# Kernel optimization log

Hardware: AMD Instinct MI355X
Metric: run time of the kernel (lower is better)

Reference implementation:

```python
import jax, jax.numpy as jnp
import numpy as np

B, D_IN, H, DIM, K = 16384, 2000, 500, 64, 256
DELTA = -5.0


def _xavier(key, shape):
    fan_out, fan_in = shape
    lim = jnp.sqrt(6.0 / (fan_in + fan_out))
    return jax.random.uniform(key, shape, jnp.float32, -lim, lim)


def setup_inputs() -> dict:
    key = jax.random.key(0)
    ks = jax.random.split(key, 8)
    return {
        "epoch": 0,
        "pre_iter": 0,
        "x": jax.random.uniform(ks[0], (B, D_IN), jnp.float32),
        "mu": jax.random.normal(ks[1], (K, DIM), jnp.float32),
        "enc_w1": _xavier(ks[2], (H, D_IN)), "enc_b1": jnp.zeros((H,), jnp.float32),
        "enc_w2": _xavier(ks[3], (DIM, H)), "enc_b2": jnp.zeros((DIM,), jnp.float32),
        "fc0_w": _xavier(ks[4], (DIM, 2 * DIM)), "fc0_b": jnp.zeros((DIM,), jnp.float32),
        "dec_w1": _xavier(ks[5], (H, DIM)), "dec_b1": jnp.zeros((H,), jnp.float32),
        "dec_w2": _xavier(ks[6], (D_IN, H)), "dec_b2": jnp.zeros((D_IN,), jnp.float32),
    }


def reference(epoch, pre_iter, x, mu, enc_w1, enc_b1, enc_w2, enc_b2,
              fc0_w, fc0_b, dec_w1, dec_b1, dec_w2, dec_b2):
    # encoder (Dropout is identity in eval)
    h = jax.nn.relu(x @ enc_w1.T + enc_b1)            # [B, 500]
    z = h @ enc_w2.T + enc_b2                          # [B, dim]
    # Stein_IMG clustering step (mu is detached in the original)
    mu_d = jax.lax.stop_gradient(mu)
    diff = z[:, None, :] - mu_d[None, :, :]           # [B, K, dim]
    z_dist = jnp.mean(diff * diff, axis=2)            # [B, K]
    gamma = jax.nn.softmax(DELTA * z_dist, axis=1)    # [B, K]
    idx = jnp.argmax(gamma, axis=1)                   # [B]
    # one-hot scatter + matmul with mu == gather of nearest centroid
    quantized = mu_d[idx]                             # [B, dim]
    double_z = jnp.concatenate([z, quantized], axis=1)  # [B, 2*dim]
    recon_z = double_z @ fc0_w.T + fc0_b              # [B, dim]
    # decoder
    h2 = jax.nn.relu(recon_z @ dec_w1.T + dec_b1)     # [B, 500]
    recon_x = jax.nn.sigmoid(h2 @ dec_w2.T + dec_b2)  # [B, 2000]
    return (z, quantized, gamma, recon_x)
```

## Files before the change

kernel.cpp:

```cpp
#include <hip/hip_runtime.h>
#include <stdint.h>
#include <math.h>

#define NB   16384
#define DIN  2000
#define NH   500
#define ND   64
#define NKC  256

#define FLAG_CAP 4096
#define GAP_THR  0.002f

typedef __attribute__((ext_vector_type(4))) float  f32x4;
typedef __attribute__((ext_vector_type(4))) double f64x4;
typedef __attribute__((ext_vector_type(8))) short  s16x8;

__device__ __forceinline__ unsigned short f2bf_rne(float v) {
  unsigned int u = __float_as_uint(v);
  u += 0x7fffu + ((u >> 16) & 1u);
  return (unsigned short)(u >> 16);
}
__device__ __forceinline__ void split_rtz(float v, unsigned short &hi, unsigned short &lo) {
  unsigned int u = __float_as_uint(v);
  hi = (unsigned short)(u >> 16);
  float r = v - __uint_as_float(u & 0xffff0000u);
  lo = (unsigned short)(__float_as_uint(r) >> 16);
}

typedef const __attribute__((address_space(1))) void* gas_t;
typedef __attribute__((address_space(3))) void* las_t;
__device__ __forceinline__ void gl_lds16(const void* g, void* l) {
  __builtin_amdgcn_global_load_lds((gas_t)g, (las_t)l, 16, 0, 0);
}

__device__ __forceinline__ void split_pad_seg(const float* __restrict__ in,
                                              unsigned short* __restrict__ hi,
                                              unsigned short* __restrict__ lo,
                                              int R, int C, int Cp, int total,
                                              int bseg, int nblk) {
  int stride = nblk * 256;
  for (int idx = bseg * 256 + threadIdx.x; idx < total; idx += stride) {
    int r = idx / Cp, c = idx - r * Cp;
    float v = (r < R && c < C) ? in[(size_t)r * C + c] : 0.f;
    if (lo) {
      unsigned short h, l; split_rtz(v, h, l);
      hi[idx] = h; lo[idx] = l;
    } else {
      hi[idx] = f2bf_rne(v);
    }
  }
}

__global__ __launch_bounds__(256) void k_prep(const float* __restrict__ x,
                                              unsigned short* __restrict__ XHI,
                                              unsigned short* __restrict__ XLO,
                                              const float* __restrict__ w1,
                                              unsigned short* __restrict__ W1HI,
                                              unsigned short* __restrict__ W1LO,
                                              const float* __restrict__ w2,
                                              unsigned short* __restrict__ W2HI,
                                              unsigned short* __restrict__ W2LO,
                                              const float* __restrict__ dw1,
                                              unsigned short* __restrict__ DW1,
                                              const float* __restrict__ dw2,
                                              unsigned short* __restrict__ DW2,
                                              int* __restrict__ fcnt)
{
  const int b = blockIdx.x;
  if (b == 0 && threadIdx.x == 0) *fcnt = 0;
  if (b < 2048) {
    const int total = NB * 256;
    for (int idx = b * 256 + threadIdx.x; idx < total; idx += 2048 * 256) {
      int r = idx >> 8;
      int c8 = (idx & 255) << 3;
      s16x8 h8 = {0,0,0,0,0,0,0,0}, l8 = {0,0,0,0,0,0,0,0};
      if (c8 < DIN) {
        const float* src = x + (size_t)r * DIN + c8;
        f32x4 v0 = *(const f32x4*)src;
        f32x4 v1 = *(const f32x4*)(src + 4);
#pragma unroll
        for (int j = 0; j < 4; ++j) {
          unsigned short h, l;
          split_rtz(v0[j], h, l); h8[j] = (short)h; l8[j] = (short)l;
          split_rtz(v1[j], h, l); h8[4 + j] = (short)h; l8[4 + j] = (short)l;
        }
      }
      *(s16x8*)&XHI[(size_t)idx * 8] = h8;
      *(s16x8*)&XLO[(size_t)idx * 8] = l8;
    }
  } else if (b < 3072) {
    split_pad_seg(w1, W1HI, W1LO, 500, 2000, 2048, 512 * 2048, b - 2048, 1024);
  } else if (b < 3136) {
    split_pad_seg(w2, W2HI, W2LO, 64, 500, 512, 64 * 512, b - 3072, 64);
  } else if (b < 3200) {
    split_pad_seg(dw1, DW1, nullptr, 500, 64, 64, 512 * 64, b - 3136, 64);
  } else {
    split_pad_seg(dw2, DW2, nullptr, 2000, 500, 512, 2048 * 512, b - 3200, 896);
  }
}

template<int WR, int BN, int WC, bool SPLIT, int EPI>
__global__ __launch_bounds__(256) void k_gemm(
    const unsigned short* __restrict__ Ahi, const unsigned short* __restrict__ Alo,
    const unsigned short* __restrict__ Bhi, const unsigned short* __restrict__ Blo,
    const float* __restrict__ bias, int bias_n,
    void* __restrict__ out0, void* __restrict__ out1,
    int ldA, int K, int out_ld, int store_n)
{
  constexpr int BM = WR * 32, BK = 32;
  constexpr int ACH = BM * 4;
  constexpr int BCH = BN * 4;
  __shared__ unsigned short aHi[BM * BK];
  __shared__ unsigned short aLo[SPLIT ? BM * BK : 8];
  __shared__ unsigned short bHi[BN * BK];
  __shared__ unsigned short bLo[SPLIT ? BN * BK : 8];

  const int tid  = threadIdx.x;
  const int lane = tid & 63, wave = tid >> 6;
  const int wm = wave >> 1, wn = wave & 1;
  const int lr = lane & 15, lg = lane >> 4;
  const int swz = (lr >> 1) & 3;
  const int m0 = blockIdx.x * BM, n0 = blockIdx.y * BN;

  f32x4 acc[WR][WC];
#pragma unroll
  for (int i = 0; i < WR; ++i)
#pragma unroll
    for (int j = 0; j < WC; ++j)
#pragma unroll
      for (int r = 0; r < 4; ++r) acc[i][j][r] = 0.f;

  for (int k0 = 0; k0 < K; k0 += BK) {
#pragma unroll
    for (int j = 0; j < ACH / 256; ++j) {
      int c = (j * 4 + wave) * 64 + lane;
      int row = c >> 2;
      int ch = (c & 3) ^ ((row >> 1) & 3);
      const unsigned short* sA = Ahi + (size_t)(m0 + row) * ldA + k0 + ch * 8;
      gl_lds16(sA, (char*)aHi + c * 16);
      if constexpr (SPLIT) {
        const unsigned short* sL = Alo + (size_t)(m0 + row) * ldA + k0 + ch * 8;
        gl_lds16(sL, (char*)aLo + c * 16);
      }
    }
#pragma unroll
    for (int j = 0; j < BCH / 256; ++j) {
      int c = (j * 4 + wave) * 64 + lane;
      int row = c >> 2;
      int ch = (c & 3) ^ ((row >> 1) & 3);
      const unsigned short* sB = Bhi + (size_t)(n0 + row) * K + k0 + ch * 8;
      gl_lds16(sB, (char*)bHi + c * 16);
      if constexpr (SPLIT) {
        const unsigned short* sL = Blo + (size_t)(n0 + row) * K + k0 + ch * 8;
        gl_lds16(sL, (char*)bLo + c * 16);
      }
    }
    __syncthreads();

    const int fch = (lg ^ swz) << 3;
    s16x8 ah[WR], bh[WC];
#pragma unroll
    for (int i = 0; i < WR; ++i)
      ah[i] = *(const s16x8*)&aHi[(wm * (WR * 16) + i * 16 + lr) * 32 + fch];
#pragma unroll
    for (int j = 0; j < WC; ++j)
      bh[j] = *(const s16x8*)&bHi[(wn * (WC * 16) + j * 16 + lr) * 32 + fch];
    if constexpr (SPLIT) {
      s16x8 al[WR], bl[WC];
#pragma unroll
      for (int i = 0; i < WR; ++i)
        al[i] = *(const s16x8*)&aLo[(wm * (WR * 16) + i * 16 + lr) * 32 + fch];
#pragma unroll
      for (int j = 0; j < WC; ++j)
        bl[j] = *(const s16x8*)&bLo[(wn * (WC * 16) + j * 16 + lr) * 32 + fch];
#pragma unroll
      for (int i = 0; i < WR; ++i)
#pragma unroll
        for (int j = 0; j < WC; ++j) {
          acc[i][j] = __builtin_amdgcn_mfma_f32_16x16x32_bf16(ah[i], bh[j], acc[i][j], 0, 0, 0);
          acc[i][j] = __builtin_amdgcn_mfma_f32_16x16x32_bf16(ah[i], bl[j], acc[i][j], 0, 0, 0);
          acc[i][j] = __builtin_amdgcn_mfma_f32_16x16x32_bf16(al[i], bh[j], acc[i][j], 0, 0, 0);
        }
    } else {
#pragma unroll
      for (int i = 0; i < WR; ++i)
#pragma unroll
        for (int j = 0; j < WC; ++j)
          acc[i][j] = __builtin_amdgcn_mfma_f32_16x16x32_bf16(ah[i], bh[j], acc[i][j], 0, 0, 0);
    }
    __syncthreads();
  }

#pragma unroll
  for (int i = 0; i < WR; ++i) {
    int grow = m0 + wm * (WR * 16) + i * 16 + lg * 4;
#pragma unroll
    for (int j = 0; j < WC; ++j) {
      int gcol = n0 + wn * (WC * 16) + j * 16 + lr;
      float bv = (gcol < bias_n) ? bias[gcol] : 0.f;
      f32x4 v = acc[i][j];
#pragma unroll
      for (int r = 0; r < 4; ++r) {
        float val = v[r] + bv;
        int rr = grow + r;
        if constexpr (EPI == 0) {
          if (gcol < store_n) ((float*)out0)[(size_t)rr * out_ld + gcol] = val;
        } else if constexpr (EPI == 1) {
          val = fmaxf(val, 0.f);
          unsigned short h, l; split_rtz(val, h, l);
          ((unsigned short*)out0)[(size_t)rr * out_ld + gcol] = h;
          ((unsigned short*)out1)[(size_t)rr * out_ld + gcol] = l;
        } else if constexpr (EPI == 2) {
          val = fmaxf(val, 0.f);
          ((unsigned short*)out0)[(size_t)rr * out_ld + gcol] = f2bf_rne(val);
        } else {
          val = 1.f / (1.f + expf(-val));
          if (gcol < store_n) ((float*)out0)[(size_t)rr * out_ld + gcol] = val;
        }
      }
    }
  }
}

__global__ __launch_bounds__(256) void k_cluster(const float* __restrict__ z,
                                                 const float* __restrict__ mu,
                                                 float* __restrict__ gamma,
                                                 float* __restrict__ quant,
                                                 int* __restrict__ flag_cnt,
                                                 int* __restrict__ flag_list)
{
  __shared__ float mu_t[ND][NKC];
  for (int i = threadIdx.x; i < NKC * ND; i += 256) {
    int k = i >> 6, d = i & 63;
    mu_t[d][k] = mu[i];
  }
  __syncthreads();
  const int lane = threadIdx.x & 63, wave = threadIdx.x >> 6;
  for (int r4 = blockIdx.x * 16 + wave * 4; r4 < NB; r4 += gridDim.x * 16) {
    float zr[4];
#pragma unroll
    for (int r = 0; r < 4; ++r) zr[r] = z[(size_t)(r4 + r) * ND + lane];
    float ds[4][4];
#pragma unroll
    for (int r = 0; r < 4; ++r)
#pragma unroll
      for (int g = 0; g < 4; ++g) ds[r][g] = 0.f;
    for (int d = 0; d < ND; ++d) {
      f32x4 m4 = *(const f32x4*)&mu_t[d][lane << 2];
#pragma unroll
      for (int r = 0; r < 4; ++r) {
        float zd = __shfl(zr[r], d, 64);
#pragma unroll
        for (int g = 0; g < 4; ++g) {
          float t = zd - m4[g];
          ds[r][g] = fmaf(t, t, ds[r][g]);
        }
      }
    }
#pragma unroll
    for (int r = 0; r < 4; ++r) {
      int row = r4 + r;
      float bd = ds[r][0]; int bk = (lane << 2);
#pragma unroll
      for (int g = 1; g < 4; ++g)
        if (ds[r][g] < bd) { bd = ds[r][g]; bk = (lane << 2) + g; }
      for (int off = 1; off < 64; off <<= 1) {
        float od = __shfl_xor(bd, off, 64);
        int   ok = __shfl_xor(bk, off, 64);
        if (od < bd || (od == bd && ok < bk)) { bd = od; bk = ok; }
      }
      float sb = 3.4e38f;
#pragma unroll
      for (int g = 0; g < 4; ++g) {
        int kk = (lane << 2) + g;
        if (kk != bk) sb = fminf(sb, ds[r][g]);
      }
      for (int off = 1; off < 64; off <<= 1) sb = fminf(sb, __shfl_xor(sb, off, 64));
      if (lane == 0 && (sb - bd) < GAP_THR) {
        int p = atomicAdd(flag_cnt, 1);
        if (p < FLAG_CAP) flag_list[p] = row;
      }
      const float cc = -5.f / 64.f;
      float e[4], s = 0.f;
#pragma unroll
      for (int g = 0; g < 4; ++g) { e[g] = expf(cc * (ds[r][g] - bd)); s += e[g]; }
      for (int off = 1; off < 64; off <<= 1) s += __shfl_xor(s, off, 64);
      float inv = 1.f / s;
      f32x4 g4 = { e[0] * inv, e[1] * inv, e[2] * inv, e[3] * inv };
      *(f32x4*)&gamma[(size_t)row * NKC + (lane << 2)] = g4;
      quant[(size_t)row * ND + lane] = mu[(size_t)bk * ND + lane];
    }
  }
}

__global__ __launch_bounds__(512) void k_ref_h(const float* __restrict__ x,
                                               const float* __restrict__ w1,
                                               const float* __restrict__ b1,
                                               const int* __restrict__ flag_cnt,
                                               const int* __restrict__ flag_list,
                                               double* __restrict__ Hd)
{
  __shared__ __align__(16) double xs[2][DIN];
  __shared__ int rows_s[2];

  int cnt = *flag_cnt; if (cnt > FLAG_CAP) cnt = FLAG_CAP;
  const int base = blockIdx.x * 2;
  if (base >= cnt) return;
  const int tid = threadIdx.x, lane = tid & 63, wave = tid >> 6;
  const int ybase = blockIdx.y * 64;
  const int yend  = (ybase + 64 < NH) ? (ybase + 64) : NH;

  if (tid < 2) rows_s[tid] = flag_list[(base + tid < cnt) ? (base + tid) : base];
  __syncthreads();
  const int row0 = rows_s[0], row1 = rows_s[1];

  for (int c = tid; c < DIN; c += 512) {
    xs[0][c] = (double)x[(size_t)row0 * DIN + c];
    xs[1][c] = (double)x[(size_t)row1 * DIN + c];
  }
  __syncthreads();

  for (int hr0 = ybase + wave * 4; hr0 < yend; hr0 += 32) {
    double a[4][2];
#pragma unroll
    for (int r = 0; r < 4; ++r) { a[r][0] = 0.0; a[r][1] = 0.0; }
    for (int c = lane; c < DIN / 4; c += 64) {
      f64x4 x0 = *(const f64x4*)(&xs[0][c * 4]);
      f64x4 x1 = *(const f64x4*)(&xs[1][c * 4]);
#pragma unroll
      for (int r = 0; r < 4; ++r) {
        f32x4 w4 = *(const f32x4*)(w1 + (size_t)(hr0 + r) * DIN + c * 4);
#pragma unroll
        for (int j = 0; j < 4; ++j) {
          double w = (double)w4[j];
          a[r][0] = fma(w, x0[j], a[r][0]);
          a[r][1] = fma(w, x1[j], a[r][1]);
        }
      }
    }
#pragma unroll
    for (int off = 32; off; off >>= 1)
#pragma unroll
      for (int r = 0; r < 4; ++r) {
        a[r][0] += __shfl_xor(a[r][0], off, 64);
        a[r][1] += __shfl_xor(a[r][1], off, 64);
      }
    if (lane == 0) {
#pragma unroll
      for (int r = 0; r < 4; ++r) {
        double b = (double)b1[hr0 + r];
        double v0 = a[r][0] + b, v1 = a[r][1] + b;
        Hd[(size_t)(base + 0) * 512 + hr0 + r] = v0 > 0.0 ? v0 : 0.0;
        Hd[(size_t)(base + 1) * 512 + hr0 + r] = v1 > 0.0 ? v1 : 0.0;
      }
    }
  }
}

__global__ __launch_bounds__(512) void k_ref_zq(const float* __restrict__ w2,
                                                const float* __restrict__ b2,
                                                const float* __restrict__ mu,
                                                const double* __restrict__ Hd,
                                                const int* __restrict__ flag_cnt,
                                                const int* __restrict__ flag_list,
                                                float* __restrict__ quant)
{
  __shared__ double hsl[8][NH];
  __shared__ float  mu_t[ND][NKC + 1];
  __shared__ double zs[8][ND];
  __shared__ int    rows_s[8];

  int cnt = *flag_cnt; if (cnt > FLAG_CAP) cnt = FLAG_CAP;
  const int base = blockIdx.x * 8;
  if (base >= cnt) return;
  const int tid = threadIdx.x, lane = tid & 63, wave = tid >> 6;

  if (tid < 8) rows_s[tid] = flag_list[(base + tid < cnt) ? (base + tid) : base];
  for (int i = tid; i < NKC * ND; i += 512) {
    mu_t[i & 63][i >> 6] = mu[i];
  }
  {
    int pos = (base + wave < cnt) ? (base + wave) : base;
    const double* hr = Hd + (size_t)pos * 512;
    for (int i = lane; i < NH; i += 64) hsl[wave][i] = hr[i];
  }
  __syncthreads();

  for (int g4 = 0; g4 < 16; ++g4) {
    double a[4] = {0.0, 0.0, 0.0, 0.0};
    int q[4];
#pragma unroll
    for (int u = 0; u < 4; ++u) q[u] = g4 * 32 + u * 8 + wave;
    for (int i = lane; i < NH; i += 64) {
#pragma unroll
      for (int u = 0; u < 4; ++u) {
        int r = q[u] >> 6, d = q[u] & 63;
        a[u] = fma(hsl[r][i], (double)w2[(size_t)d * NH + i], a[u]);
      }
    }
#pragma unroll
    for (int off = 32; off; off >>= 1)
#pragma unroll
      for (int u = 0; u < 4; ++u) a[u] += __shfl_xor(a[u], off, 64);
    if (lane == 0) {
#pragma unroll
      for (int u = 0; u < 4; ++u) {
        int r = q[u] >> 6, d = q[u] & 63;
        zs[r][d] = a[u] + (double)b2[d];
      }
    }
  }
  __syncthreads();

  {
    double bd = 1.0e300; int bk = 0;
#pragma unroll
    for (int g = 0; g < 4; ++g) {
      int k = g * 64 + lane;
      double dist = 0.0;
#pragma unroll 8
      for (int d = 0; d < ND; ++d) {
        double t = zs[wave][d] - (double)mu_t[d][k];
        dist = fma(t, t, dist);
      }
      if (g == 0 || dist < bd) { bd = dist; bk = k; }
    }
    for (int off = 1; off < 64; off <<= 1) {
      double od = __shfl_xor(bd, off, 64);
      int    ok = __shfl_xor(bk, off, 64);
      if (od < bd || (od == bd && ok < bk)) { bd = od; bk = ok; }
    }
    quant[(size_t)rows_s[wave] * ND + lane] = mu[(size_t)bk * ND + lane];
  }
}

__global__ __launch_bounds__(256) void k_fc0(const float* __restrict__ z, const float* __restrict__ quant,
                                             const float* __restrict__ W, const float* __restrict__ b,
                                             unsigned short* __restrict__ rz)
{
  __shared__ float Wt[2 * ND][ND];
  for (int i = threadIdx.x; i < ND * 2 * ND; i += 256) {
    int j = i >> 7;
    int ii = i & 127;
    Wt[ii][j] = W[i];
  }
  __syncthreads();
  const int lane = threadIdx.x & 63, wave = threadIdx.x >> 6;
  float bj = b[lane];
  for (int row = blockIdx.x * 4 + wave; row < NB; row += gridDim.x * 4) {
    float zv = z[(size_t)row * ND + lane];
    float qv = quant[(size_t)row * ND + lane];
    float acc = bj;
#pragma unroll 8
    for (int i = 0; i < ND; ++i) {
      acc = fmaf(__shfl(zv, i, 64), Wt[i][lane], acc);
      acc = fmaf(__shfl(qv, i, 64), Wt[ND + i][lane], acc);
    }
    rz[(size_t)row * ND + lane] = f2bf_rne(acc);
  }
}

extern "C" void kernel_launch(void* const* d_in, const int* in_sizes, int n_in,
                              void* d_out, int out_size, void* d_ws, size_t ws_size,
                              hipStream_t stream)
{
  const float* x      = (const float*)d_in[2];
  const float* mu     = (const float*)d_in[3];
  const float* enc_w1 = (const float*)d_in[4];
  const float* enc_b1 = (const float*)d_in[5];
  const float* enc_w2 = (const float*)d_in[6];
  const float* enc_b2 = (const float*)d_in[7];
  const float* fc0_w  = (const float*)d_in[8];
  const float* fc0_b  = (const float*)d_in[9];
  const float* dec_w1 = (const float*)d_in[10];
  const float* dec_b1 = (const float*)d_in[11];
  const float* dec_w2 = (const float*)d_in[12];
  const float* dec_b2 = (const float*)d_in[13];

  float* z_out  = (float*)d_out;
  float* q_out  = z_out + (size_t)NB * ND;
  float* g_out  = q_out + (size_t)NB * ND;
  float* rx_out = g_out + (size_t)NB * NKC;

  char* ws = (char*)d_ws;
  unsigned short* XHI  = (unsigned short*)ws; ws += (size_t)NB * 2048 * 2;
  unsigned short* XLO  = (unsigned short*)ws; ws += (size_t)NB * 2048 * 2;
  unsigned short* W1HI = (unsigned short*)ws; ws += (size_t)512 * 2048 * 2;
  unsigned short* W1LO = (unsigned short*)ws; ws += (size_t)512 * 2048 * 2;
  unsigned short* W2HI = (unsigned short*)ws; ws += (size_t)64 * 512 * 2;
  unsigned short* W2LO = (unsigned short*)ws; ws += (size_t)64 * 512 * 2;
  unsigned short* DW1  = (unsigned short*)ws; ws += (size_t)512 * 64 * 2;
  unsigned short* DW2  = (unsigned short*)ws; ws += (size_t)2048 * 512 * 2;
  unsigned short* HHI  = (unsigned short*)ws; ws += (size_t)NB * 512 * 2;
  unsigned short* HLO  = (unsigned short*)ws; ws += (size_t)NB * 512 * 2;
  unsigned short* H2   = (unsigned short*)ws; ws += (size_t)NB * 512 * 2;
  unsigned short* RZ   = (unsigned short*)ws; ws += (size_t)NB * ND * 2;
  int* FCNT = (int*)ws; ws += 256;
  int* FLST = (int*)ws; ws += (size_t)FLAG_CAP * 4;
  double* Hd = (double*)XHI;

  k_prep<<<4096, 256, 0, stream>>>(x, XHI, XLO, enc_w1, W1HI, W1LO,
                                   enc_w2, W2HI, W2LO, dec_w1, DW1, dec_w2, DW2, FCNT);

  dim3 g1(NB / 128, 4);
  k_gemm<4, 128, 4, true, 1><<<g1, 256, 0, stream>>>(
      XHI, XLO, W1HI, W1LO, enc_b1, 500, HHI, HLO, 2048, 2048, 512, 512);
  dim3 g2(NB / 64, 1);
  k_gemm<2, 64, 2, true, 0><<<g2, 256, 0, stream>>>(
      HHI, HLO, W2HI, W2LO, enc_b2, 64, z_out, nullptr, 512, 512, 64, 64);
  k_cluster<<<256, 256, 0, stream>>>(z_out, mu, g_out, q_out, FCNT, FLST);
  dim3 gh(FLAG_CAP / 2, 8);
  k_ref_h<<<gh, 512, 0, stream>>>(x, enc_w1, enc_b1, FCNT, FLST, Hd);
  k_ref_zq<<<FLAG_CAP / 8, 512, 0, stream>>>(enc_w2, enc_b2, mu, Hd, FCNT, FLST, q_out);
  k_fc0<<<256, 256, 0, stream>>>(z_out, q_out, fc0_w, fc0_b, RZ);
  dim3 g4(NB / 128, 4);
  k_gemm<4, 128, 4, false, 2><<<g4, 256, 0, stream>>>(
      RZ, nullptr, DW1, nullptr, dec_b1, 500, H2, nullptr, 64, 64, 512, 512);
  dim3 g5(NB / 128, 16);
  k_gemm<4, 128, 4, false, 3><<<g5, 256, 0, stream>>>(
      H2, nullptr, DW2, nullptr, dec_b2, 2000, rx_out, nullptr, 512, 512, 2000, 2000);
}
```

Before: 423.4 us.

## Fuse fp32-to-bf16 hi/lo split of x into first encoder GEMM load

The first encoder GEMM now reads x directly in fp32 and splits each value into bf16 hi/lo parts while staging its A tile into LDS. This removes the separate prep pass that wrote the XHI/XLO split copies of x to memory. The goal is to cut that round trip through global memory. In exchange, the A tile is loaded synchronously through registers instead of async global-to-LDS copies, and the wider fp32 data is re-read by each of the four column blocks. The reference hidden buffer gets its own workspace slot instead of aliasing XHI.

```diff
diff --git a/kernel.cpp b/kernel.cpp
--- a/kernel.cpp
+++ b/kernel.cpp
@@ -51,10 +51,7 @@
   }
 }
 
-__global__ __launch_bounds__(256) void k_prep(const float* __restrict__ x,
-                                              unsigned short* __restrict__ XHI,
-                                              unsigned short* __restrict__ XLO,
-                                              const float* __restrict__ w1,
+__global__ __launch_bounds__(256) void k_prep(const float* __restrict__ w1,
                                               unsigned short* __restrict__ W1HI,
                                               unsigned short* __restrict__ W1LO,
                                               const float* __restrict__ w2,
@@ -68,40 +65,21 @@
 {
   const int b = blockIdx.x;
   if (b == 0 && threadIdx.x == 0) *fcnt = 0;
-  if (b < 2048) {
-    const int total = NB * 256;
-    for (int idx = b * 256 + threadIdx.x; idx < total; idx += 2048 * 256) {
-      int r = idx >> 8;
-      int c8 = (idx & 255) << 3;
-      s16x8 h8 = {0,0,0,0,0,0,0,0}, l8 = {0,0,0,0,0,0,0,0};
-      if (c8 < DIN) {
-        const float* src = x + (size_t)r * DIN + c8;
-        f32x4 v0 = *(const f32x4*)src;
-        f32x4 v1 = *(const f32x4*)(src + 4);
-#pragma unroll
-        for (int j = 0; j < 4; ++j) {
-          unsigned short h, l;
-          split_rtz(v0[j], h, l); h8[j] = (short)h; l8[j] = (short)l;
-          split_rtz(v1[j], h, l); h8[4 + j] = (short)h; l8[4 + j] = (short)l;
-        }
-      }
-      *(s16x8*)&XHI[(size_t)idx * 8] = h8;
-      *(s16x8*)&XLO[(size_t)idx * 8] = l8;
-    }
-  } else if (b < 3072) {
-    split_pad_seg(w1, W1HI, W1LO, 500, 2000, 2048, 512 * 2048, b - 2048, 1024);
-  } else if (b < 3136) {
-    split_pad_seg(w2, W2HI, W2LO, 64, 500, 512, 64 * 512, b - 3072, 64);
-  } else if (b < 3200) {
-    split_pad_seg(dw1, DW1, nullptr, 500, 64, 64, 512 * 64, b - 3136, 64);
+  if (b < 1024) {
+    split_pad_seg(w1, W1HI, W1LO, 500, 2000, 2048, 512 * 2048, b, 1024);
+  } else if (b < 1088) {
+    split_pad_seg(w2, W2HI, W2LO, 64, 500, 512, 64 * 512, b - 1024, 64);
+  } else if (b < 1152) {
+    split_pad_seg(dw1, DW1, nullptr, 500, 64, 64, 512 * 64, b - 1088, 64);
   } else {
-    split_pad_seg(dw2, DW2, nullptr, 2000, 500, 512, 2048 * 512, b - 3200, 896);
-  }
-}
-
-template<int WR, int BN, int WC, bool SPLIT, int EPI>
+    split_pad_seg(dw2, DW2, nullptr, 2000, 500, 512, 2048 * 512, b - 1152, 896);
+  }
+}
+
+template<int WR, int BN, int WC, bool SPLIT, bool AF32, int EPI>
 __global__ __launch_bounds__(256) void k_gemm(
     const unsigned short* __restrict__ Ahi, const unsigned short* __restrict__ Alo,
+    const float* __restrict__ Axf,
     const unsigned short* __restrict__ Bhi, const unsigned short* __restrict__ Blo,
     const float* __restrict__ bias, int bias_n,
     void* __restrict__ out0, void* __restrict__ out1,
@@ -136,11 +114,29 @@
       int c = (j * 4 + wave) * 64 + lane;
       int row = c >> 2;
       int ch = (c & 3) ^ ((row >> 1) & 3);
-      const unsigned short* sA = Ahi + (size_t)(m0 + row) * ldA + k0 + ch * 8;
-      gl_lds16(sA, (char*)aHi + c * 16);
-      if constexpr (SPLIT) {
-        const unsigned short* sL = Alo + (size_t)(m0 + row) * ldA + k0 + ch * 8;
-        gl_lds16(sL, (char*)aLo + c * 16);
+      if constexpr (AF32) {
+        int col = k0 + ch * 8;
+        s16x8 h8 = {0,0,0,0,0,0,0,0}, l8 = {0,0,0,0,0,0,0,0};
+        if (col < DIN) {
+          const float* src = Axf + (size_t)(m0 + row) * ldA + col;
+          f32x4 v0 = *(const f32x4*)src;
+          f32x4 v1 = *(const f32x4*)(src + 4);
+#pragma unroll
+          for (int q = 0; q < 4; ++q) {
+            unsigned short h, l;
+            split_rtz(v0[q], h, l); h8[q] = (short)h; l8[q] = (short)l;
+            split_rtz(v1[q], h, l); h8[4 + q] = (short)h; l8[4 + q] = (short)l;
+          }
+        }
+        *(s16x8*)&aHi[c * 8] = h8;
+        *(s16x8*)&aLo[c * 8] = l8;
+      } else {
+        const unsigned short* sA = Ahi + (size_t)(m0 + row) * ldA + k0 + ch * 8;
+        gl_lds16(sA, (char*)aHi + c * 16);
+        if constexpr (SPLIT) {
+          const unsigned short* sL = Alo + (size_t)(m0 + row) * ldA + k0 + ch * 8;
+          gl_lds16(sL, (char*)aLo + c * 16);
+        }
       }
     }
 #pragma unroll
@@ -483,8 +479,6 @@
   float* rx_out = g_out + (size_t)NB * NKC;
 
   char* ws = (char*)d_ws;
-  unsigned short* XHI  = (unsigned short*)ws; ws += (size_t)NB * 2048 * 2;
-  unsigned short* XLO  = (unsigned short*)ws; ws += (size_t)NB * 2048 * 2;
   unsigned short* W1HI = (unsigned short*)ws; ws += (size_t)512 * 2048 * 2;
   unsigned short* W1LO = (unsigned short*)ws; ws += (size_t)512 * 2048 * 2;
   unsigned short* W2HI = (unsigned short*)ws; ws += (size_t)64 * 512 * 2;
@@ -497,26 +491,26 @@
   unsigned short* RZ   = (unsigned short*)ws; ws += (size_t)NB * ND * 2;
   int* FCNT = (int*)ws; ws += 256;
   int* FLST = (int*)ws; ws += (size_t)FLAG_CAP * 4;
-  double* Hd = (double*)XHI;
-
-  k_prep<<<4096, 256, 0, stream>>>(x, XHI, XLO, enc_w1, W1HI, W1LO,
-                                   enc_w2, W2HI, W2LO, dec_w1, DW1, dec_w2, DW2, FCNT);
+  double* Hd = (double*)ws; ws += (size_t)FLAG_CAP * 512 * 8;
+
+  k_prep<<<2048, 256, 0, stream>>>(enc_w1, W1HI, W1LO, enc_w2, W2HI, W2LO,
+                                   dec_w1, DW1, dec_w2, DW2, FCNT);
 
   dim3 g1(NB / 128, 4);
-  k_gemm<4, 128, 4, true, 1><<<g1, 256, 0, stream>>>(
-      XHI, XLO, W1HI, W1LO, enc_b1, 500, HHI, HLO, 2048, 2048, 512, 512);
+  k_gemm<4, 128, 4, true, true, 1><<<g1, 256, 0, stream>>>(
+      nullptr, nullptr, x, W1HI, W1LO, enc_b1, 500, HHI, HLO, DIN, 2048, 512, 512);
   dim3 g2(NB / 64, 1);
-  k_gemm<2, 64, 2, true, 0><<<g2, 256, 0, stream>>>(
-      HHI, HLO, W2HI, W2LO, enc_b2, 64, z_out, nullptr, 512, 512, 64, 64);
+  k_gemm<2, 64, 2, true, false, 0><<<g2, 256, 0, stream>>>(
+      HHI, HLO, nullptr, W2HI, W2LO, enc_b2, 64, z_out, nullptr, 512, 512, 64, 64);
   k_cluster<<<256, 256, 0, stream>>>(z_out, mu, g_out, q_out, FCNT, FLST);
   dim3 gh(FLAG_CAP / 2, 8);
   k_ref_h<<<gh, 512, 0, stream>>>(x, enc_w1, enc_b1, FCNT, FLST, Hd);
   k_ref_zq<<<FLAG_CAP / 8, 512, 0, stream>>>(enc_w2, enc_b2, mu, Hd, FCNT, FLST, q_out);
   k_fc0<<<256, 256, 0, stream>>>(z_out, q_out, fc0_w, fc0_b, RZ);
   dim3 g4(NB / 128, 4);
-  k_gemm<4, 128, 4, false, 2><<<g4, 256, 0, stream>>>(
-      RZ, nullptr, DW1, nullptr, dec_b1, 500, H2, nullptr, 64, 64, 512, 512);
+  k_gemm<4, 128, 4, false, false, 2><<<g4, 256, 0, stream>>>(
+      RZ, nullptr, nullptr, DW1, nullptr, dec_b1, 500, H2, nullptr, 64, 64, 512, 512);
   dim3 g5(NB / 128, 16);
-  k_gemm<4, 128, 4, false, 3><<<g5, 256, 0, stream>>>(
-      H2, nullptr, DW2, nullptr, dec_b2, 2000, rx_out, nullptr, 512, 512, 2000, 2000);
-}
+  k_gemm<4, 128, 4, false, false, 3><<<g5, 256, 0, stream>>>(
+      H2, nullptr, nullptr, DW2, nullptr, dec_b2, 2000, rx_out, nullptr, 512, 512, 2000, 2000);
+}
```

Measured after the change: 378.8 us. -10.5%, faster.
